# Optimization experiments

Hardware: AMD Instinct MI355X
Metric: run time of the kernel (lower is better)

Reference implementation:

```python
import jax, jax.numpy as jnp
import numpy as np

JUMP_THRESHOLD = 0.5
BLEND = 0.7  # blend_factor in original


def _phase_corrected(x):
    # x: [B, C, T], C even; first half channels = magnitude, second = normalized phase
    half = x.shape[1] // 2
    magnitude = x[:, :half]
    phase_norm = x[:, half:]

    # phase_grad[t] = phase[t] - phase[t-1], with grad[0] = 0 (as in torch code)
    grad = jnp.concatenate(
        [jnp.zeros_like(phase_norm[:, :, :1]), phase_norm[:, :, 1:] - phase_norm[:, :, :-1]],
        axis=2,
    )
    jumps = jnp.abs(grad) > JUMP_THRESHOLD
    # The original O(T) python loop subtracts sign(grad[j]) from all positions >= j+1
    # whenever jumps[j]; equivalently a right-shifted cumulative sum of corrections.
    d = jnp.where(jumps, jnp.sign(grad), jnp.zeros_like(grad))
    corr = jnp.cumsum(d, axis=2)
    corr = jnp.concatenate([jnp.zeros_like(corr[:, :, :1]), corr[:, :, :-1]], axis=2)
    phase_smooth = phase_norm - corr

    phase = phase_smooth * (2.0 * jnp.pi) - jnp.pi

    # F.avg_pool1d(kernel=3, stride=1, padding=1) with count_include_pad=True:
    # zero-pad and divide by 3 everywhere (including edges).
    p = jnp.pad(phase, ((0, 0), (0, 0), (1, 1)))
    phase_smoothed = (p[:, :, :-2] + p[:, :, 1:-1] + p[:, :, 2:]) * (1.0 / 3.0)

    phase_final = BLEND * phase + (1.0 - BLEND) * phase_smoothed
    real_part = magnitude * jnp.cos(phase_final)
    imag_part = magnitude * jnp.sin(phase_final)
    return real_part, imag_part


def setup_inputs() -> dict:
    key = jax.random.key(0)
    x = jax.random.normal(key, (16, 128, 16384), dtype=jnp.float32)
    return {"x": x}


def reference(x):
    real_part, imag_part = _phase_corrected(x)
    return jax.lax.complex(real_part, imag_part)
```

## Files before the change

kernel.cpp:

```cpp
#include <hip/hip_runtime.h>
#include <math.h>

#define N_T    16384
#define BLOCK  1024
#define NCH    4
#define CHSZ   4096
#define NWAVE  16

template <int MODE>
__global__ __launch_bounds__(BLOCK)
void phase_kernel(const float* __restrict__ x, float* __restrict__ out) {
    __shared__ float rawEdge[NCH][NWAVE];
    __shared__ int   wtot[NCH][NWAVE];
    __shared__ float corrR[NCH][NWAVE];
    __shared__ float corrL[NCH][NWAVE];

    const int tid  = threadIdx.x;
    const int lane = tid & 63;
    const int wv   = tid >> 6;
    const int r    = blockIdx.x;
    const int b    = r >> 6;
    const int c    = r & 63;
    const float* __restrict__ phase_row = x + ((size_t)(b * 128 + 64 + c)) * N_T;
    const float* __restrict__ mag_row   = x + ((size_t)(b * 128 + c)) * N_T;

    const float TWO_PI = 6.28318530717958647692f;
    const float PI_F   = 3.14159265358979323846f;
    const float THIRD  = 1.0f / 3.0f;

    float s[16];
    #pragma unroll
    for (int i = 0; i < NCH; ++i) {
        float4 v = *reinterpret_cast<const float4*>(phase_row + i * CHSZ + tid * 4);
        s[i * 4 + 0] = v.x; s[i * 4 + 1] = v.y;
        s[i * 4 + 2] = v.z; s[i * 4 + 3] = v.w;
    }

    if (lane == 63) {
        #pragma unroll
        for (int i = 0; i < NCH; ++i) rawEdge[i][wv] = s[i * 4 + 3];
    }
    __syncthreads();

    float prevRaw[NCH];
    #pragma unroll
    for (int i = 0; i < NCH; ++i) {
        float p = __shfl_up(s[i * 4 + 3], 1);
        if (lane == 0) {
            if (wv > 0)      p = rawEdge[i][wv - 1];
            else if (i > 0)  p = rawEdge[i - 1][NWAVE - 1];
            else             p = 0.0f;
        }
        prevRaw[i] = p;
    }

    int lsum[NCH];
    #pragma unroll
    for (int i = 0; i < NCH; ++i) {
        float prev = prevRaw[i];
        int cnt = 0;
        #pragma unroll
        for (int k = 0; k < 4; ++k) {
            float cur = s[i * 4 + k];
            float g = cur - prev;
            bool first = (i == 0 && tid == 0 && k == 0);
            if (!first && fabsf(g) > 0.5f) cnt += (g > 0.0f) ? 1 : -1;
            prev = cur;
        }
        lsum[i] = cnt;
    }

    int incl[NCH] = {lsum[0], lsum[1], lsum[2], lsum[3]};
    #pragma unroll
    for (int off = 1; off < 64; off <<= 1) {
        #pragma unroll
        for (int i = 0; i < NCH; ++i) {
            int n = __shfl_up(incl[i], off);
            if (lane >= off) incl[i] += n;
        }
    }
    if (lane == 63) {
        #pragma unroll
        for (int i = 0; i < NCH; ++i) wtot[i][wv] = incl[i];
    }
    __syncthreads();

    int P[NCH];
    {
        int chunkPre = 0;
        #pragma unroll
        for (int i = 0; i < NCH; ++i) {
            int wpre = 0, tot = 0;
            #pragma unroll
            for (int w = 0; w < NWAVE; ++w) {
                int t = wtot[i][w];
                if (w < wv) wpre += t;
                tot += t;
            }
            P[i] = chunkPre + wpre + (incl[i] - lsum[i]);
            chunkPre += tot;
        }
    }

    #pragma unroll
    for (int i = 0; i < NCH; ++i) {
        int running = P[i];
        float prev = prevRaw[i];
        #pragma unroll
        for (int k = 0; k < 4; ++k) {
            float cur = s[i * 4 + k];
            int d = 0;
            bool first = (i == 0 && tid == 0 && k == 0);
            if (!first) {
                float g = cur - prev;
                if (fabsf(g) > 0.5f) d = (g > 0.0f) ? 1 : -1;
            }
            s[i * 4 + k] = (cur - (float)running) * TWO_PI - PI_F;
            running += d;
            prev = cur;
        }
    }

    if (lane == 63) {
        #pragma unroll
        for (int i = 0; i < NCH; ++i) corrR[i][wv] = s[i * 4 + 3];
    }
    if (lane == 0) {
        #pragma unroll
        for (int i = 0; i < NCH; ++i) corrL[i][wv] = s[i * 4 + 0];
    }
    float4 mg[NCH];
    #pragma unroll
    for (int i = 0; i < NCH; ++i)
        mg[i] = *reinterpret_cast<const float4*>(mag_row + i * CHSZ + tid * 4);
    __syncthreads();

    #pragma unroll
    for (int i = 0; i < NCH; ++i) {
        float left = __shfl_up(s[i * 4 + 3], 1);
        if (lane == 0) {
            if (wv > 0)      left = corrR[i][wv - 1];
            else if (i > 0)  left = corrR[i - 1][NWAVE - 1];
            else             left = 0.0f;
        }
        float right = __shfl_down(s[i * 4 + 0], 1);
        if (lane == 63) {
            if (wv < NWAVE - 1)  right = corrL[i][wv + 1];
            else if (i < NCH - 1) right = corrL[i + 1][0];
            else                  right = 0.0f;
        }

        float mgk[4] = {mg[i].x, mg[i].y, mg[i].z, mg[i].w};
        float re[4], im[4];
        #pragma unroll
        for (int k = 0; k < 4; ++k) {
            float pm = (k == 0) ? left  : s[i * 4 + k - 1];
            float pp = (k == 3) ? right : s[i * 4 + k + 1];
            float cur = s[i * 4 + k];
            float sm = ((pm + cur) + pp) * THIRD;
            float pf = 0.7f * cur + 0.3f * sm;
            float nrev = rintf(pf * 0.15915494309189535f);
            float rr = fmaf(nrev, -6.28318548202514648f, pf);
            rr = fmaf(nrev, 1.74845553e-7f, rr);
            re[k] = mgk[k] * __cosf(rr);
            if (MODE == 1) im[k] = mgk[k] * __sinf(rr);
        }
        if (MODE == 0) {
            float* o = out + (size_t)r * N_T + i * CHSZ + tid * 4;
            *reinterpret_cast<float4*>(o) = make_float4(re[0], re[1], re[2], re[3]);
        } else {
            float* o = out + (size_t)r * (2 * N_T) + 2 * (i * CHSZ + tid * 4);
            *reinterpret_cast<float4*>(o)     = make_float4(re[0], im[0], re[1], im[1]);
            *reinterpret_cast<float4*>(o + 4) = make_float4(re[2], im[2], re[3], im[3]);
        }
    }
}

extern "C" void kernel_launch(void* const* d_in, const int* in_sizes, int n_in,
                              void* d_out, int out_size, void* d_ws, size_t ws_size,
                              hipStream_t stream) {
    const float* x = (const float*)d_in[0];
    float* out = (float*)d_out;
    int n_rows = in_sizes[0] / (2 * N_T);
    if (out_size >= in_sizes[0]) {
        phase_kernel<1><<<n_rows, BLOCK, 0, stream>>>(x, out);
    } else {
        phase_kernel<0><<<n_rows, BLOCK, 0, stream>>>(x, out);
    }
}
```

Measured before the change: 36.05 us.

## Split each row across four blocks with redundant prefix jump counting

```diff
diff --git a/kernel.cpp b/kernel.cpp
--- a/kernel.cpp
+++ b/kernel.cpp
@@ -1,28 +1,40 @@
 #include <hip/hip_runtime.h>
 #include <math.h>
 
-#define N_T    16384
-#define BLOCK  1024
-#define NCH    4
-#define CHSZ   4096
-#define NWAVE  16
+#define N_T   16384
+#define BLOCK 256
+#define CHSZ  4096
+#define SUB   1024
+#define NSUB  4
+#define NWAVE 4
+#define CPR   4
 
 template <int MODE>
 __global__ __launch_bounds__(BLOCK)
-void phase_kernel(const float* __restrict__ x, float* __restrict__ out) {
-    __shared__ float rawEdge[NCH][NWAVE];
-    __shared__ int   wtot[NCH][NWAVE];
-    __shared__ float corrR[NCH][NWAVE];
-    __shared__ float corrL[NCH][NWAVE];
+void phase_kernel(const float* __restrict__ x, float* __restrict__ out,
+                  int n_rows) {
+    __shared__ float rawEdge[NSUB][NWAVE];
+    __shared__ int   wtot[NSUB][NWAVE];
+    __shared__ float corrR[NSUB][NWAVE];
+    __shared__ float corrL[NSUB][NWAVE];
+    __shared__ int   preSum[NWAVE];
 
     const int tid  = threadIdx.x;
     const int lane = tid & 63;
     const int wv   = tid >> 6;
-    const int r    = blockIdx.x;
-    const int b    = r >> 6;
-    const int c    = r & 63;
-    const float* __restrict__ phase_row = x + ((size_t)(b * 128 + 64 + c)) * N_T;
-    const float* __restrict__ mag_row   = x + ((size_t)(b * 128 + c)) * N_T;
+    const int bid  = blockIdx.x;
+    int cpos = 0;
+    {
+        int t = bid;
+        if (t >= 2 * n_rows) { cpos += 2; t -= 2 * n_rows; }
+        if (t >= n_rows)     { cpos += 1; t -= n_rows; }
+    }
+    const int row = bid - cpos * n_rows;
+    const int b   = row >> 6;
+    const int c   = row & 63;
+    const float* __restrict__ row_ph   = x + ((size_t)(b * 128 + 64 + c)) * N_T;
+    const float* __restrict__ chunk_ph = row_ph + cpos * CHSZ;
+    const float* __restrict__ chunk_mg = x + ((size_t)(b * 128 + c)) * N_T + cpos * CHSZ;
 
     const float TWO_PI = 6.28318530717958647692f;
     const float PI_F   = 3.14159265358979323846f;
@@ -30,87 +42,116 @@
 
     float s[16];
     #pragma unroll
-    for (int i = 0; i < NCH; ++i) {
-        float4 v = *reinterpret_cast<const float4*>(phase_row + i * CHSZ + tid * 4);
+    for (int i = 0; i < NSUB; ++i) {
+        float4 v = *reinterpret_cast<const float4*>(chunk_ph + i * SUB + tid * 4);
         s[i * 4 + 0] = v.x; s[i * 4 + 1] = v.y;
         s[i * 4 + 2] = v.z; s[i * 4 + 3] = v.w;
     }
+    float leftRaw = 0.0f, leftRaw2 = 0.0f, rightRaw = 0.0f;
+    if (tid == 0 && cpos > 0)        { leftRaw = chunk_ph[-1]; leftRaw2 = chunk_ph[-2]; }
+    if (tid == BLOCK - 1 && cpos < CPR - 1) rightRaw = chunk_ph[CHSZ];
+
+    if (cpos > 0) {
+        const int L     = cpos * SUB;
+        const int start = wv * L;
+        float carry = 0.0f;
+        if (lane == 0 && start > 0) carry = row_ph[start - 1];
+        carry = __shfl(carry, 0);
+        const bool first0 = (start == 0);
+        int cnt = 0;
+        for (int it = 0; it < cpos * 4; ++it) {
+            float4 v = *reinterpret_cast<const float4*>(row_ph + start + it * 256 + lane * 4);
+            float up   = __shfl_up(v.w, 1);
+            float prev = (lane == 0) ? carry : up;
+            float g0 = v.x - prev, g1 = v.y - v.x, g2 = v.z - v.y, g3 = v.w - v.z;
+            bool first = first0 && it == 0 && lane == 0;
+            if (!first && fabsf(g0) > 0.5f) cnt += (g0 > 0.0f) ? 1 : -1;
+            if (fabsf(g1) > 0.5f)           cnt += (g1 > 0.0f) ? 1 : -1;
+            if (fabsf(g2) > 0.5f)           cnt += (g2 > 0.0f) ? 1 : -1;
+            if (fabsf(g3) > 0.5f)           cnt += (g3 > 0.0f) ? 1 : -1;
+            carry = __shfl(v.w, 63);
+        }
+        #pragma unroll
+        for (int off = 32; off; off >>= 1) cnt += __shfl_xor(cnt, off);
+        if (lane == 0) preSum[wv] = cnt;
+    }
 
     if (lane == 63) {
         #pragma unroll
-        for (int i = 0; i < NCH; ++i) rawEdge[i][wv] = s[i * 4 + 3];
+        for (int i = 0; i < NSUB; ++i) rawEdge[i][wv] = s[i * 4 + 3];
     }
     __syncthreads();
 
-    float prevRaw[NCH];
-    #pragma unroll
-    for (int i = 0; i < NCH; ++i) {
+    int pre = 0;
+    if (cpos > 0) pre = preSum[0] + preSum[1] + preSum[2] + preSum[3];
+
+    float prevRaw[NSUB];
+    #pragma unroll
+    for (int i = 0; i < NSUB; ++i) {
         float p = __shfl_up(s[i * 4 + 3], 1);
         if (lane == 0) {
             if (wv > 0)      p = rawEdge[i][wv - 1];
             else if (i > 0)  p = rawEdge[i - 1][NWAVE - 1];
-            else             p = 0.0f;
+            else             p = leftRaw;
         }
         prevRaw[i] = p;
     }
 
-    int lsum[NCH];
-    #pragma unroll
-    for (int i = 0; i < NCH; ++i) {
+    int lsum[NSUB];
+    #pragma unroll
+    for (int i = 0; i < NSUB; ++i) {
         float prev = prevRaw[i];
         int cnt = 0;
         #pragma unroll
         for (int k = 0; k < 4; ++k) {
             float cur = s[i * 4 + k];
             float g = cur - prev;
-            bool first = (i == 0 && tid == 0 && k == 0);
+            bool first = (cpos == 0 && i == 0 && tid == 0 && k == 0);
             if (!first && fabsf(g) > 0.5f) cnt += (g > 0.0f) ? 1 : -1;
             prev = cur;
         }
         lsum[i] = cnt;
     }
 
-    int incl[NCH] = {lsum[0], lsum[1], lsum[2], lsum[3]};
+    int incl[NSUB] = {lsum[0], lsum[1], lsum[2], lsum[3]};
     #pragma unroll
     for (int off = 1; off < 64; off <<= 1) {
         #pragma unroll
-        for (int i = 0; i < NCH; ++i) {
+        for (int i = 0; i < NSUB; ++i) {
             int n = __shfl_up(incl[i], off);
             if (lane >= off) incl[i] += n;
         }
     }
     if (lane == 63) {
         #pragma unroll
-        for (int i = 0; i < NCH; ++i) wtot[i][wv] = incl[i];
+        for (int i = 0; i < NSUB; ++i) wtot[i][wv] = incl[i];
     }
     __syncthreads();
 
-    int P[NCH];
-    {
-        int chunkPre = 0;
-        #pragma unroll
-        for (int i = 0; i < NCH; ++i) {
-            int wpre = 0, tot = 0;
-            #pragma unroll
-            for (int w = 0; w < NWAVE; ++w) {
-                int t = wtot[i][w];
-                if (w < wv) wpre += t;
-                tot += t;
-            }
-            P[i] = chunkPre + wpre + (incl[i] - lsum[i]);
-            chunkPre += tot;
-        }
-    }
-
-    #pragma unroll
-    for (int i = 0; i < NCH; ++i) {
+    int P[NSUB];
+    int chunkPre = pre;
+    #pragma unroll
+    for (int i = 0; i < NSUB; ++i) {
+        int wpre = 0, tot = 0;
+        #pragma unroll
+        for (int w = 0; w < NWAVE; ++w) {
+            int t = wtot[i][w];
+            if (w < wv) wpre += t;
+            tot += t;
+        }
+        P[i] = chunkPre + wpre + (incl[i] - lsum[i]);
+        chunkPre += tot;
+    }
+
+    #pragma unroll
+    for (int i = 0; i < NSUB; ++i) {
         int running = P[i];
         float prev = prevRaw[i];
         #pragma unroll
         for (int k = 0; k < 4; ++k) {
             float cur = s[i * 4 + k];
             int d = 0;
-            bool first = (i == 0 && tid == 0 && k == 0);
+            bool first = (cpos == 0 && i == 0 && tid == 0 && k == 0);
             if (!first) {
                 float g = cur - prev;
                 if (fabsf(g) > 0.5f) d = (g > 0.0f) ? 1 : -1;
@@ -121,33 +162,45 @@
         }
     }
 
+    float v_left = 0.0f, v_right = 0.0f;
+    if (tid == 0 && cpos > 0) {
+        float g = leftRaw - leftRaw2;
+        int d = (fabsf(g) > 0.5f) ? ((g > 0.0f) ? 1 : -1) : 0;
+        int corr = pre - d;
+        v_left = (leftRaw - (float)corr) * TWO_PI - PI_F;
+    }
+    if (tid == BLOCK - 1 && cpos < CPR - 1) {
+        int corr = chunkPre;
+        v_right = (rightRaw - (float)corr) * TWO_PI - PI_F;
+    }
+
     if (lane == 63) {
         #pragma unroll
-        for (int i = 0; i < NCH; ++i) corrR[i][wv] = s[i * 4 + 3];
+        for (int i = 0; i < NSUB; ++i) corrR[i][wv] = s[i * 4 + 3];
     }
     if (lane == 0) {
         #pragma unroll
-        for (int i = 0; i < NCH; ++i) corrL[i][wv] = s[i * 4 + 0];
-    }
-    float4 mg[NCH];
-    #pragma unroll
-    for (int i = 0; i < NCH; ++i)
-        mg[i] = *reinterpret_cast<const float4*>(mag_row + i * CHSZ + tid * 4);
+        for (int i = 0; i < NSUB; ++i) corrL[i][wv] = s[i * 4 + 0];
+    }
+    float4 mg[NSUB];
+    #pragma unroll
+    for (int i = 0; i < NSUB; ++i)
+        mg[i] = *reinterpret_cast<const float4*>(chunk_mg + i * SUB + tid * 4);
     __syncthreads();
 
     #pragma unroll
-    for (int i = 0; i < NCH; ++i) {
+    for (int i = 0; i < NSUB; ++i) {
         float left = __shfl_up(s[i * 4 + 3], 1);
         if (lane == 0) {
             if (wv > 0)      left = corrR[i][wv - 1];
             else if (i > 0)  left = corrR[i - 1][NWAVE - 1];
-            else             left = 0.0f;
+            else             left = v_left;
         }
         float right = __shfl_down(s[i * 4 + 0], 1);
         if (lane == 63) {
-            if (wv < NWAVE - 1)  right = corrL[i][wv + 1];
-            else if (i < NCH - 1) right = corrL[i + 1][0];
-            else                  right = 0.0f;
+            if (wv < NWAVE - 1)   right = corrL[i][wv + 1];
+            else if (i < NSUB - 1) right = corrL[i + 1][0];
+            else                   right = v_right;
         }
 
         float mgk[4] = {mg[i].x, mg[i].y, mg[i].z, mg[i].w};
@@ -166,10 +219,10 @@
             if (MODE == 1) im[k] = mgk[k] * __sinf(rr);
         }
         if (MODE == 0) {
-            float* o = out + (size_t)r * N_T + i * CHSZ + tid * 4;
+            float* o = out + (size_t)row * N_T + cpos * CHSZ + i * SUB + tid * 4;
             *reinterpret_cast<float4*>(o) = make_float4(re[0], re[1], re[2], re[3]);
         } else {
-            float* o = out + (size_t)r * (2 * N_T) + 2 * (i * CHSZ + tid * 4);
+            float* o = out + (size_t)row * (2 * N_T) + 2 * (cpos * CHSZ + i * SUB + tid * 4);
             *reinterpret_cast<float4*>(o)     = make_float4(re[0], im[0], re[1], im[1]);
             *reinterpret_cast<float4*>(o + 4) = make_float4(re[2], im[2], re[3], im[3]);
         }
@@ -182,9 +235,10 @@
     const float* x = (const float*)d_in[0];
     float* out = (float*)d_out;
     int n_rows = in_sizes[0] / (2 * N_T);
+    int grid = n_rows * CPR;
     if (out_size >= in_sizes[0]) {
-        phase_kernel<1><<<n_rows, BLOCK, 0, stream>>>(x, out);
+        phase_kernel<1><<<grid, BLOCK, 0, stream>>>(x, out, n_rows);
     } else {
-        phase_kernel<0><<<n_rows, BLOCK, 0, stream>>>(x, out);
+        phase_kernel<0><<<grid, BLOCK, 0, stream>>>(x, out, n_rows);
     }
 }
```

Measured after the change: 48.84 us. 1.35x slower.
